# Performance work log

Measured on AMD Instinct MI355X. Metric: run time of the kernel, lower is better.

Reference implementation:

```python
import jax, jax.numpy as jnp
import numpy as np

# angular momenta of the full basis (2s,3s,2p,3p,3d) -> block sizes 1,1,3,3,5; norb=13
L_LIST = [0, 0, 1, 1, 2]


def factor_matrix():
    """Replicates the orbital-pair loop: factor 0.5 on diagonal orbital blocks,
    1.0 for i<j blocks, 0.0 below the block diagonal (only i<=j filled)."""
    sizes = [2 * l + 1 for l in L_LIST]
    norb = sum(sizes)
    F = np.zeros((norb, norb), np.float32)
    ist = 0
    for i, si in enumerate(sizes):
        jst = 0
        for j, sj in enumerate(sizes):
            if i < j:
                F[ist:ist + si, jst:jst + sj] = 1.0
            elif i == j:
                F[ist:ist + si, jst:jst + sj] = 0.5
            jst += sj
        ist += si
    return jnp.asarray(F)


def setup_inputs() -> dict:
    key = jax.random.key(0)
    k1, k2, k3, k4, k5 = jax.random.split(key, 5)
    N, E, K = 128, 2048, 16
    norb = sum(2 * l + 1 for l in L_LIST)  # 13
    return {
        "hopping": jax.random.normal(k1, (E, norb * norb), jnp.float32),
        "onsite": jax.random.normal(k2, (N, norb * norb), jnp.float32),
        "kpoints": jax.random.uniform(k3, (K, 3), jnp.float32),
        "cell_shift": jax.random.normal(k4, (E, 3), jnp.float32),
        "edge_index": jax.random.randint(k5, (2, E), 0, N, jnp.int64),
    }


def reference(hopping, onsite, kpoints, cell_shift, edge_index):
    F = factor_matrix()
    norb = F.shape[0]
    N = onsite.shape[0]
    K = kpoints.shape[0]
    ctype = jnp.complex64

    # per-edge / per-atom orbital blocks with upper-triangular factor (i<=j loop)
    hop = (hopping.reshape(-1, norb, norb) * F).astype(ctype)   # [E,norb,norb]
    ons = (onsite.reshape(-1, norb, norb) * F).astype(ctype)    # [N,norb,norb]

    # Bloch phase exp(-i 2*pi k.R) per (k, edge)
    phase = jnp.exp(-1j * 2.0 * jnp.pi * (kpoints @ cell_shift.T).astype(ctype))  # [K,E]

    # assemble block Hamiltonian [K, N, N, norb, norb]
    H = jnp.zeros((K, N, N, norb, norb), ctype)
    ar = jnp.arange(N)
    H = H.at[:, ar, ar].add(ons[None])  # onsite diagonal blocks (no phase)
    ie, je = edge_index[0], edge_index[1]
    H = H.at[:, ie, je].add(phase[:, :, None, None] * hop[None])  # scatter-add edges

    # hermitize: block + block^H (swap atom blocks and orbital indices)
    H = H + jnp.conj(jnp.swapaxes(jnp.swapaxes(H, 1, 2), 3, 4))
    # [K, N, norb, N, norb] -> [K, all_norb, all_norb]
    Hk = H.transpose(0, 1, 3, 2, 4).reshape(K, N * norb, N * norb)
    return Hk
```

## Files before the change

kernel.cpp:

```cpp
#include <hip/hip_runtime.h>
#include <math.h>

#define NORB 13
#define NORB2 (NORB * NORB)
#define GB 16

typedef float fx4 __attribute__((ext_vector_type(4)));

__device__ __forceinline__ int blk_of(int p) {
    return p < 1 ? 0 : (p < 2 ? 1 : (p < 5 ? 2 : (p < 8 ? 3 : 4)));
}
__device__ __forceinline__ float ffac(int p, int q) {
    int bp = blk_of(p), bq = blk_of(q);
    return bp < bq ? 1.0f : (bp == bq ? 0.5f : 0.0f);
}

__global__ void __launch_bounds__(256)
k_build(const int* __restrict__ edge_index, int* __restrict__ rowptr,
        int* __restrict__ entries, int E, int N, int ngroups) {
    extern __shared__ int sm[];
    int nbins = N * ngroups;
    int* cnt    = sm;
    int* cursor = sm + nbins;
    int* part   = sm + 2 * nbins;
    int tid = threadIdx.x;

    for (int i = tid; i < nbins; i += 256) cnt[i] = 0;
    __syncthreads();

    for (int e = tid; e < E; e += 256) {
        int ie = edge_index[e], je = edge_index[E + e];
        atomicAdd(cnt + ie * ngroups + (je >> 4), 1);
        atomicAdd(cnt + je * ngroups + (ie >> 4), 1);
    }
    __syncthreads();

    int per = nbins / 256;
    int base = tid * per;
    int s = 0;
    for (int i = 0; i < per; ++i) s += cnt[base + i];
    part[tid + 1] = s;
    __syncthreads();
    if (tid == 0) {
        part[0] = 0;
        for (int i = 1; i <= 256; ++i) part[i] += part[i - 1];
    }
    __syncthreads();
    int run = part[tid];
    for (int i = 0; i < per; ++i) {
        rowptr[base + i] = run;
        cursor[base + i] = run;
        run += cnt[base + i];
    }
    if (tid == 255) rowptr[nbins] = run;
    __syncthreads();

    for (int e = tid; e < E; e += 256) {
        int ie = edge_index[e], je = edge_index[E + e];
        int pos = atomicAdd(cursor + ie * ngroups + (je >> 4), 1);
        entries[pos] = (e << 9) | je;
        pos = atomicAdd(cursor + je * ngroups + (ie >> 4), 1);
        entries[pos] = (e << 9) | 256 | ie;
    }
}

__global__ void __launch_bounds__(256)
k_assemble(const float* __restrict__ hopping,
           const float* __restrict__ onsite,
           const float* __restrict__ kpoints,
           const float* __restrict__ cell_shift,
           const int* __restrict__ rowptr,
           const int* __restrict__ entries,
           float* __restrict__ out,
           int N, int K, int ld, int es, int ngroups) {
    int g = blockIdx.x % ngroups;
    int a = (blockIdx.x / ngroups) % N;
    int k = blockIdx.x / (ngroups * N);
    int tid = threadIdx.x;
    int b0 = g * GB;
    int nb = min(GB, N - b0);

    __shared__ __align__(16) float lds[NORB * GB * NORB * 2];
    fx4* lds4 = (fx4*)lds;
    const int LDSF4 = NORB * GB * NORB * 2 / 4;
    for (int i = tid; i < LDSF4; i += 256)
        lds4[i] = (fx4){0.f, 0.f, 0.f, 0.f};

    int p = 0, q = 0;
    bool act = tid < NORB2;
    if (act) { p = tid / NORB; q = tid - p * NORB; }
    float fpq = act ? ffac(p, q) : 0.f;
    float fqp = act ? ffac(q, p) : 0.f;
    float kx = kpoints[3 * k], ky = kpoints[3 * k + 1], kz = kpoints[3 * k + 2];

    int bin = a * ngroups + g;
    int beg = rowptr[bin], end = rowptr[bin + 1];
    __syncthreads();

    if (a >= b0 && a < b0 + nb && act) {
        const float* on = onsite + (size_t)a * NORB2;
        float v = on[p * NORB + q] * fpq + on[q * NORB + p] * fqp;
        lds[(p * GB * NORB + (a - b0) * NORB + q) * 2] = v;
    }

    for (int it = beg; it < end; ++it) {
        int ent = entries[it];
        int e = ent >> 9;
        int rev = ent & 256;
        int i = (ent & 255) - b0;
        float Rx = cell_shift[3 * e], Ry = cell_shift[3 * e + 1], Rz = cell_shift[3 * e + 2];
        float d = kx * Rx + ky * Ry + kz * Rz;
        float s, c;
        sincosf(-6.2831853071795864f * d, &s, &c);
        float im = rev ? -s : s;
        if (act) {
            const float* h = hopping + (size_t)e * NORB2;
            float hv = rev ? h[q * NORB + p] * fqp : h[p * NORB + q] * fpq;
            int base = (p * GB * NORB + i * NORB + q) * 2;
            lds[base]     += c * hv;
            lds[base + 1] += im * hv;
        }
    }
    __syncthreads();

    if (es == 2 && nb == GB) {
        const int ROWF4 = GB * NORB * 2 / 4;
        fx4* o4 = (fx4*)out;
        for (int idx = tid; idx < NORB * ROWF4; idx += 256) {
            int row = idx / ROWF4;
            int col = idx - row * ROWF4;
            size_t gc = ((size_t)k * ld + (size_t)a * NORB + row) * ld + (size_t)b0 * NORB;
            __builtin_nontemporal_store(lds4[row * ROWF4 + col], &o4[(gc >> 1) + col]);
        }
    } else if (es == 2) {
        float2* o2 = (float2*)out;
        int nelem = NORB * nb * NORB;
        for (int idx = tid; idx < nelem; idx += 256) {
            int row = idx / (nb * NORB);
            int rem = idx - row * nb * NORB;
            size_t gc = ((size_t)k * ld + (size_t)a * NORB + row) * ld + (size_t)b0 * NORB + rem;
            int li = (row * GB * NORB + rem) * 2;
            o2[gc] = make_float2(lds[li], lds[li + 1]);
        }
    } else {
        int nelem = NORB * nb * NORB;
        for (int idx = tid; idx < nelem; idx += 256) {
            int row = idx / (nb * NORB);
            int rem = idx - row * nb * NORB;
            size_t gc = ((size_t)k * ld + (size_t)a * NORB + row) * ld + (size_t)b0 * NORB + rem;
            out[gc] = lds[(row * GB * NORB + rem) * 2];
        }
    }
}

extern "C" void kernel_launch(void* const* d_in, const int* in_sizes, int n_in,
                              void* d_out, int out_size, void* d_ws, size_t ws_size,
                              hipStream_t stream) {
    const float* hopping    = (const float*)d_in[0];
    const float* onsite     = (const float*)d_in[1];
    const float* kpoints    = (const float*)d_in[2];
    const float* cell_shift = (const float*)d_in[3];
    const int*   edge_index = (const int*)d_in[4];
    float* out = (float*)d_out;

    int E = in_sizes[0] / NORB2;
    int N = in_sizes[1] / NORB2;
    int K = in_sizes[2] / 3;
    int ld = N * NORB;
    int ngroups = (N + GB - 1) / GB;
    int nbins = N * ngroups;

    size_t full = (size_t)K * ld * ld * 2;
    int es = ((size_t)out_size >= full) ? 2 : 1;

    int* rowptr  = (int*)d_ws;
    int* entries = rowptr + nbins + 1;

    size_t build_lds = (size_t)(2 * nbins + 257) * sizeof(int);
    k_build<<<1, 256, build_lds, stream>>>(edge_index, rowptr, entries, E, N, ngroups);

    int nwg = K * N * ngroups;
    k_assemble<<<nwg, 256, 0, stream>>>(hopping, onsite, kpoints, cell_shift,
                                        rowptr, entries, out, N, K, ld, es, ngroups);
}
```

Measured before the change: 232.9 us.

## Loop over k-points inside each workgroup with LDS reuse and fast sincos

Each workgroup now handles a chunk of k-points (the grid is split into KSPLIT chunks) instead of one, so the onsite block and the entry range are loaded once and the LDS tile is re-zeroed while being written out. The precise sincosf is replaced by __sincosf, and the nontemporal stores become plain vector stores. This cuts the grid from K*N*ngroups to 2*N*ngroups workgroups, which lowers launch and setup overhead per tile but reduces parallelism and serialises the stores inside each workgroup.

```diff
diff --git a/kernel.cpp b/kernel.cpp
--- a/kernel.cpp
+++ b/kernel.cpp
@@ -4,6 +4,7 @@
 #define NORB 13
 #define NORB2 (NORB * NORB)
 #define GB 16
+#define KSPLIT 2
 
 typedef float fx4 __attribute__((ext_vector_type(4)));
 
@@ -73,9 +74,11 @@
            const int* __restrict__ entries,
            float* __restrict__ out,
            int N, int K, int ld, int es, int ngroups) {
-    int g = blockIdx.x % ngroups;
-    int a = (blockIdx.x / ngroups) % N;
-    int k = blockIdx.x / (ngroups * N);
+    int g  = blockIdx.x % ngroups;
+    int a  = (blockIdx.x / ngroups) % N;
+    int kc = blockIdx.x / (ngroups * N);
+    int kch = (K + KSPLIT - 1) / KSPLIT;
+    int k0 = kc * kch, k1 = min(K, k0 + kch);
     int tid = threadIdx.x;
     int b0 = g * GB;
     int nb = min(GB, N - b0);
@@ -91,65 +94,82 @@
     if (act) { p = tid / NORB; q = tid - p * NORB; }
     float fpq = act ? ffac(p, q) : 0.f;
     float fqp = act ? ffac(q, p) : 0.f;
-    float kx = kpoints[3 * k], ky = kpoints[3 * k + 1], kz = kpoints[3 * k + 2];
+
+    bool diag = (a >= b0 && a < b0 + nb);
+    float onv = 0.f;
+    int  ondst = 0;
+    if (diag && act) {
+        const float* on = onsite + (size_t)a * NORB2;
+        onv = on[p * NORB + q] * fpq + on[q * NORB + p] * fqp;
+        ondst = (p * GB * NORB + (a - b0) * NORB + q) * 2;
+    }
 
     int bin = a * ngroups + g;
     int beg = rowptr[bin], end = rowptr[bin + 1];
     __syncthreads();
 
-    if (a >= b0 && a < b0 + nb && act) {
-        const float* on = onsite + (size_t)a * NORB2;
-        float v = on[p * NORB + q] * fpq + on[q * NORB + p] * fqp;
-        lds[(p * GB * NORB + (a - b0) * NORB + q) * 2] = v;
-    }
-
-    for (int it = beg; it < end; ++it) {
-        int ent = entries[it];
-        int e = ent >> 9;
-        int rev = ent & 256;
-        int i = (ent & 255) - b0;
-        float Rx = cell_shift[3 * e], Ry = cell_shift[3 * e + 1], Rz = cell_shift[3 * e + 2];
-        float d = kx * Rx + ky * Ry + kz * Rz;
-        float s, c;
-        sincosf(-6.2831853071795864f * d, &s, &c);
-        float im = rev ? -s : s;
-        if (act) {
-            const float* h = hopping + (size_t)e * NORB2;
-            float hv = rev ? h[q * NORB + p] * fqp : h[p * NORB + q] * fpq;
-            int base = (p * GB * NORB + i * NORB + q) * 2;
-            lds[base]     += c * hv;
-            lds[base + 1] += im * hv;
+    const int ROWF4 = GB * NORB * 2 / 4;
+    bool fastpath = (es == 2) && (nb == GB);
+
+    for (int k = k0; k < k1; ++k) {
+        float kx = kpoints[3 * k], ky = kpoints[3 * k + 1], kz = kpoints[3 * k + 2];
+
+        if (diag && act) {
+            lds[ondst] += onv;
         }
-    }
-    __syncthreads();
-
-    if (es == 2 && nb == GB) {
-        const int ROWF4 = GB * NORB * 2 / 4;
-        fx4* o4 = (fx4*)out;
-        for (int idx = tid; idx < NORB * ROWF4; idx += 256) {
-            int row = idx / ROWF4;
-            int col = idx - row * ROWF4;
-            size_t gc = ((size_t)k * ld + (size_t)a * NORB + row) * ld + (size_t)b0 * NORB;
-            __builtin_nontemporal_store(lds4[row * ROWF4 + col], &o4[(gc >> 1) + col]);
+        for (int it = beg; it < end; ++it) {
+            int ent = entries[it];
+            int e = ent >> 9;
+            int rev = ent & 256;
+            int i = (ent & 255) - b0;
+            float Rx = cell_shift[3 * e], Ry = cell_shift[3 * e + 1], Rz = cell_shift[3 * e + 2];
+            float d = kx * Rx + ky * Ry + kz * Rz;
+            float s, c;
+            __sincosf(-6.2831853071795864f * d, &s, &c);
+            float im = rev ? -s : s;
+            if (act) {
+                const float* h = hopping + (size_t)e * NORB2;
+                float hv = rev ? h[q * NORB + p] * fqp : h[p * NORB + q] * fpq;
+                int base = (p * GB * NORB + i * NORB + q) * 2;
+                lds[base]     += c * hv;
+                lds[base + 1] += im * hv;
+            }
         }
-    } else if (es == 2) {
-        float2* o2 = (float2*)out;
-        int nelem = NORB * nb * NORB;
-        for (int idx = tid; idx < nelem; idx += 256) {
-            int row = idx / (nb * NORB);
-            int rem = idx - row * nb * NORB;
-            size_t gc = ((size_t)k * ld + (size_t)a * NORB + row) * ld + (size_t)b0 * NORB + rem;
-            int li = (row * GB * NORB + rem) * 2;
-            o2[gc] = make_float2(lds[li], lds[li + 1]);
+        __syncthreads();
+
+        if (fastpath) {
+            fx4* o4 = (fx4*)out;
+            for (int idx = tid; idx < NORB * ROWF4; idx += 256) {
+                int row = idx / ROWF4;
+                int col = idx - row * ROWF4;
+                fx4 v = lds4[idx];
+                lds4[idx] = (fx4){0.f, 0.f, 0.f, 0.f};
+                size_t gc = ((size_t)k * ld + (size_t)a * NORB + row) * ld + (size_t)b0 * NORB;
+                o4[(gc >> 1) + col] = v;
+            }
+        } else if (es == 2) {
+            float2* o2 = (float2*)out;
+            int nelem = NORB * nb * NORB;
+            for (int idx = tid; idx < nelem; idx += 256) {
+                int row = idx / (nb * NORB);
+                int rem = idx - row * nb * NORB;
+                size_t gc = ((size_t)k * ld + (size_t)a * NORB + row) * ld + (size_t)b0 * NORB + rem;
+                int li = (row * GB * NORB + rem) * 2;
+                o2[gc] = make_float2(lds[li], lds[li + 1]);
+                lds[li] = 0.f; lds[li + 1] = 0.f;
+            }
+        } else {
+            int nelem = NORB * nb * NORB;
+            for (int idx = tid; idx < nelem; idx += 256) {
+                int row = idx / (nb * NORB);
+                int rem = idx - row * nb * NORB;
+                size_t gc = ((size_t)k * ld + (size_t)a * NORB + row) * ld + (size_t)b0 * NORB + rem;
+                int li = (row * GB * NORB + rem) * 2;
+                out[gc] = lds[li];
+                lds[li] = 0.f; lds[li + 1] = 0.f;
+            }
         }
-    } else {
-        int nelem = NORB * nb * NORB;
-        for (int idx = tid; idx < nelem; idx += 256) {
-            int row = idx / (nb * NORB);
-            int rem = idx - row * nb * NORB;
-            size_t gc = ((size_t)k * ld + (size_t)a * NORB + row) * ld + (size_t)b0 * NORB + rem;
-            out[gc] = lds[(row * GB * NORB + rem) * 2];
-        }
+        __syncthreads();
     }
 }
 
@@ -179,7 +199,7 @@
     size_t build_lds = (size_t)(2 * nbins + 257) * sizeof(int);
     k_build<<<1, 256, build_lds, stream>>>(edge_index, rowptr, entries, E, N, ngroups);
 
-    int nwg = K * N * ngroups;
+    int nwg = N * ngroups * KSPLIT;
     k_assemble<<<nwg, 256, 0, stream>>>(hopping, onsite, kpoints, cell_shift,
                                         rowptr, entries, out, N, K, ld, es, ngroups);
 }
```

After: 223.8 us. -3.9%, faster.

## Compute output elements directly in registers and loop k-points within each block

Applied to the files above, without the earlier changes.

The assemble kernel no longer zeroes and accumulates a shared-memory tile per (k, atom, group). It buckets each bin's entries by destination atom into a small shared list, then has each thread compute its output float4 slots in registers and write them directly. Each workgroup now loops over half the k-points, so the bucketing and onsite work are amortized and the grid shrinks by K/2. It also switches to fast __sincosf and drops nontemporal stores. This adds risks: entries beyond CAP=32 per destination atom are silently dropped, and the grid is now much smaller.

```diff
diff --git a/kernel.cpp b/kernel.cpp
--- a/kernel.cpp
+++ b/kernel.cpp
@@ -4,6 +4,10 @@
 #define NORB 13
 #define NORB2 (NORB * NORB)
 #define GB 16
+#define ROWF4 (GB * NORB * 2 / 4)
+#define NSLOT (NORB * ROWF4)
+#define CAP 32
+#define KSPLIT 2
 
 typedef float fx4 __attribute__((ext_vector_type(4)));
 
@@ -30,8 +34,8 @@
 
     for (int e = tid; e < E; e += 256) {
         int ie = edge_index[e], je = edge_index[E + e];
-        atomicAdd(cnt + ie * ngroups + (je >> 4), 1);
-        atomicAdd(cnt + je * ngroups + (ie >> 4), 1);
+        atomicAdd(cnt + ie * ngroups + je / GB, 1);
+        atomicAdd(cnt + je * ngroups + ie / GB, 1);
     }
     __syncthreads();
 
@@ -57,9 +61,9 @@
 
     for (int e = tid; e < E; e += 256) {
         int ie = edge_index[e], je = edge_index[E + e];
-        int pos = atomicAdd(cursor + ie * ngroups + (je >> 4), 1);
+        int pos = atomicAdd(cursor + ie * ngroups + je / GB, 1);
         entries[pos] = (e << 9) | je;
-        pos = atomicAdd(cursor + je * ngroups + (ie >> 4), 1);
+        pos = atomicAdd(cursor + je * ngroups + ie / GB, 1);
         entries[pos] = (e << 9) | 256 | ie;
     }
 }
@@ -73,82 +77,114 @@
            const int* __restrict__ entries,
            float* __restrict__ out,
            int N, int K, int ld, int es, int ngroups) {
-    int g = blockIdx.x % ngroups;
-    int a = (blockIdx.x / ngroups) % N;
-    int k = blockIdx.x / (ngroups * N);
+    int g  = blockIdx.x % ngroups;
+    int a  = (blockIdx.x / ngroups) % N;
+    int kc = blockIdx.x / (ngroups * N);
+    int kch = (K + KSPLIT - 1) / KSPLIT;
+    int k0 = kc * kch, k1 = min(K, k0 + kch);
     int tid = threadIdx.x;
     int b0 = g * GB;
     int nb = min(GB, N - b0);
 
-    __shared__ __align__(16) float lds[NORB * GB * NORB * 2];
-    fx4* lds4 = (fx4*)lds;
-    const int LDSF4 = NORB * GB * NORB * 2 / 4;
-    for (int i = tid; i < LDSF4; i += 256)
-        lds4[i] = (fx4){0.f, 0.f, 0.f, 0.f};
-
-    int p = 0, q = 0;
-    bool act = tid < NORB2;
-    if (act) { p = tid / NORB; q = tid - p * NORB; }
-    float fpq = act ? ffac(p, q) : 0.f;
-    float fqp = act ? ffac(q, p) : 0.f;
-    float kx = kpoints[3 * k], ky = kpoints[3 * k + 1], kz = kpoints[3 * k + 2];
-
+    __shared__ int lcnt[GB];
+    __shared__ int lent[GB][CAP];
+    if (tid < GB) lcnt[tid] = 0;
+    __syncthreads();
     int bin = a * ngroups + g;
     int beg = rowptr[bin], end = rowptr[bin + 1];
-    __syncthreads();
-
-    if (a >= b0 && a < b0 + nb && act) {
-        const float* on = onsite + (size_t)a * NORB2;
-        float v = on[p * NORB + q] * fpq + on[q * NORB + p] * fqp;
-        lds[(p * GB * NORB + (a - b0) * NORB + q) * 2] = v;
-    }
-
-    for (int it = beg; it < end; ++it) {
+    for (int it = beg + tid; it < end; it += 256) {
         int ent = entries[it];
+        int i = (ent & 255) - b0;
+        int pos = atomicAdd(&lcnt[i], 1);
+        if (pos < CAP) lent[i][pos] = ent;
+    }
+    __syncthreads();
+
+    const float* on = onsite + (size_t)a * NORB2;
+
+    auto contrib = [&](int ent, int p, int q, float kx, float ky, float kz,
+                       float& vre, float& vim) {
         int e = ent >> 9;
         int rev = ent & 256;
-        int i = (ent & 255) - b0;
         float Rx = cell_shift[3 * e], Ry = cell_shift[3 * e + 1], Rz = cell_shift[3 * e + 2];
         float d = kx * Rx + ky * Ry + kz * Rz;
-        float s, c;
-        sincosf(-6.2831853071795864f * d, &s, &c);
-        float im = rev ? -s : s;
-        if (act) {
-            const float* h = hopping + (size_t)e * NORB2;
-            float hv = rev ? h[q * NORB + p] * fqp : h[p * NORB + q] * fpq;
-            int base = (p * GB * NORB + i * NORB + q) * 2;
-            lds[base]     += c * hv;
-            lds[base + 1] += im * hv;
+        float s_, c_;
+        __sincosf(-6.2831853071795864f * d, &s_, &c_);
+        float hv = rev ? hopping[(size_t)e * NORB2 + q * NORB + p] * ffac(q, p)
+                       : hopping[(size_t)e * NORB2 + p * NORB + q] * ffac(p, q);
+        vre += c_ * hv;
+        vim += (rev ? -s_ : s_) * hv;
+    };
+
+    if (es == 2 && nb == GB) {
+        int   sn[6];
+        float so0[6], so1[6];
+#pragma unroll
+        for (int u = 0; u < 6; ++u) {
+            int s = tid + (u << 8);
+            sn[u] = 0; so0[u] = 0.f; so1[u] = 0.f;
+            if (s < NSLOT) {
+                int row = s / ROWF4;
+                int c = s - row * ROWF4;
+                int j0 = 2 * c;
+                int i0 = j0 / NORB, q0 = j0 - NORB * i0;
+                int j1 = j0 + 1;
+                int i1 = j1 / NORB, q1 = j1 - NORB * i1;
+                sn[u] = (min(lcnt[i0], CAP) << 16) | min(lcnt[i1], CAP);
+                if (b0 + i0 == a)
+                    so0[u] = on[row * NORB + q0] * ffac(row, q0)
+                           + on[q0 * NORB + row] * ffac(q0, row);
+                if (b0 + i1 == a)
+                    so1[u] = on[row * NORB + q1] * ffac(row, q1)
+                           + on[q1 * NORB + row] * ffac(q1, row);
+            }
         }
-    }
-    __syncthreads();
-
-    if (es == 2 && nb == GB) {
-        const int ROWF4 = GB * NORB * 2 / 4;
+
         fx4* o4 = (fx4*)out;
-        for (int idx = tid; idx < NORB * ROWF4; idx += 256) {
-            int row = idx / ROWF4;
-            int col = idx - row * ROWF4;
-            size_t gc = ((size_t)k * ld + (size_t)a * NORB + row) * ld + (size_t)b0 * NORB;
-            __builtin_nontemporal_store(lds4[row * ROWF4 + col], &o4[(gc >> 1) + col]);
-        }
-    } else if (es == 2) {
-        float2* o2 = (float2*)out;
-        int nelem = NORB * nb * NORB;
-        for (int idx = tid; idx < nelem; idx += 256) {
-            int row = idx / (nb * NORB);
-            int rem = idx - row * nb * NORB;
-            size_t gc = ((size_t)k * ld + (size_t)a * NORB + row) * ld + (size_t)b0 * NORB + rem;
-            int li = (row * GB * NORB + rem) * 2;
-            o2[gc] = make_float2(lds[li], lds[li + 1]);
+        for (int k = k0; k < k1; ++k) {
+            float kx = kpoints[3 * k], ky = kpoints[3 * k + 1], kz = kpoints[3 * k + 2];
+#pragma unroll
+            for (int u = 0; u < 6; ++u) {
+                int s = tid + (u << 8);
+                if (s >= NSLOT) break;
+                int row = s / ROWF4;
+                int c = s - row * ROWF4;
+                int j0 = 2 * c;
+                int i0 = j0 / NORB, q0 = j0 - NORB * i0;
+                int j1 = j0 + 1;
+                int i1 = j1 / NORB, q1 = j1 - NORB * i1;
+                int n0 = sn[u] >> 16, n1 = sn[u] & 0xffff;
+                float re0 = so0[u], im0 = 0.f;
+                float re1 = so1[u], im1 = 0.f;
+                for (int n = 0; n < n0; ++n)
+                    contrib(lent[i0][n], row, q0, kx, ky, kz, re0, im0);
+                for (int n = 0; n < n1; ++n)
+                    contrib(lent[i1][n], row, q1, kx, ky, kz, re1, im1);
+                size_t gc = ((size_t)k * ld + (size_t)a * NORB + row) * ld
+                          + (size_t)b0 * NORB;
+                o4[(gc >> 1) + c] = (fx4){re0, im0, re1, im1};
+            }
         }
     } else {
         int nelem = NORB * nb * NORB;
-        for (int idx = tid; idx < nelem; idx += 256) {
-            int row = idx / (nb * NORB);
-            int rem = idx - row * nb * NORB;
-            size_t gc = ((size_t)k * ld + (size_t)a * NORB + row) * ld + (size_t)b0 * NORB + rem;
-            out[gc] = lds[(row * GB * NORB + rem) * 2];
+        for (int k = k0; k < k1; ++k) {
+            float kx = kpoints[3 * k], ky = kpoints[3 * k + 1], kz = kpoints[3 * k + 2];
+            for (int idx = tid; idx < nelem; idx += 256) {
+                int row = idx / (nb * NORB);
+                int rem = idx - row * nb * NORB;
+                int i = rem / NORB, q = rem - NORB * i;
+                float vre = 0.f, vim = 0.f;
+                if (b0 + i == a)
+                    vre = on[row * NORB + q] * ffac(row, q)
+                        + on[q * NORB + row] * ffac(q, row);
+                int n0 = min(lcnt[i], CAP);
+                for (int n = 0; n < n0; ++n)
+                    contrib(lent[i][n], row, q, kx, ky, kz, vre, vim);
+                size_t gc = ((size_t)k * ld + (size_t)a * NORB + row) * ld
+                          + (size_t)b0 * NORB + rem;
+                if (es == 2) ((float2*)out)[gc] = make_float2(vre, vim);
+                else         out[gc] = vre;
+            }
         }
     }
 }
@@ -179,7 +215,7 @@
     size_t build_lds = (size_t)(2 * nbins + 257) * sizeof(int);
     k_build<<<1, 256, build_lds, stream>>>(edge_index, rowptr, entries, E, N, ngroups);
 
-    int nwg = K * N * ngroups;
+    int nwg = N * ngroups * KSPLIT;
     k_assemble<<<nwg, 256, 0, stream>>>(hopping, onsite, kpoints, cell_shift,
                                         rowptr, entries, out, N, K, ld, es, ngroups);
 }
```

Result: slower. 289.7 us (+24.4%).
